# Performance work log

Hardware: AMD Instinct MI355X
Metric: run time of the kernel (lower is better)

Reference implementation:

```python
import jax, jax.numpy as jnp
import numpy as np

WIN_SIZE = 256           # GlobalConfig.win_size (assumed)
NFFT = 2 * WIN_SIZE      # 512 -> NFREQ = 257 rfft bins
HOP = WIN_SIZE
NFREQ = WIN_SIZE + 1
K = 3                    # all kernel sizes in the model
EPS = 1e-5


def _stft(x):
    # x: (B, S) -> (B, T, F, 2) real view of complex STFT (hann window, no center)
    B, S = x.shape
    T = (S - NFFT) // HOP + 1
    n = jnp.arange(NFFT)
    win = 0.5 - 0.5 * jnp.cos(2.0 * jnp.pi * n / NFFT)
    idx = jnp.arange(T)[:, None] * HOP + n[None, :]
    frames = x[:, idx] * win                       # (B, T, NFFT)
    spec = jnp.fft.rfft(frames, axis=-1)           # (B, T, F) complex
    return jnp.stack([spec.real, spec.imag], axis=-1).astype(x.dtype)


def _td_layer(x, W, b, same):
    # time-distributed conv over the frequency axis. x: (B,T,F,Cin), W: (k,Cin,Cout)
    k = W.shape[0]
    if same:
        x = jnp.pad(x, ((0, 0), (0, 0), (k // 2, k - 1 - k // 2), (0, 0)))
    Fout = x.shape[2] - k + 1
    xs = jnp.stack([x[:, :, i:i + Fout] for i in range(k)], axis=0)  # (k,B,T,Fout,Cin)
    return jnp.einsum('kbtfc,kco->btfo', xs, W) + b


def _td_block(x, W1, b1, W2, b2):
    h = jax.nn.relu(_td_layer(x, W1, b1, True))
    return _td_layer(h, W2, b2, True)


def _layer(x, g, beta, dw, W1, b1, W2, b2):
    # LayerNorm over (F, C), causal depthwise conv over T, TD pointwise block, ReLU
    B, T, F, C = x.shape
    mu = x.mean(axis=(-2, -1), keepdims=True)
    var = x.var(axis=(-2, -1), keepdims=True)
    xn = (x - mu) * jax.lax.rsqrt(var + EPS) * g + beta
    h = xn.reshape(B, T, F * C)
    hp = jnp.pad(h, ((0, 0), (K - 1, 0), (0, 0)))   # causal left-pad on time
    y = sum(hp[:, i:i + T, :] * dw[:, i] for i in range(K))  # (B,T,F*C) depthwise
    y = y.reshape(B, T, F, C)
    return jax.nn.relu(_td_block(y, W1, b1, W2, b2))


def setup_inputs() -> dict:
    key = jax.random.key(0)
    ks = iter(jax.random.split(key, 40))
    def rn(shape, s=0.05):
        return (jax.random.normal(next(ks), shape) * s).astype(jnp.float32)
    F = NFREQ
    d = {}
    d['x'] = jax.random.normal(next(ks), (8, 262144), dtype=jnp.float32)
    d['l0_W1'] = rn((3, 2, 4)); d['l0_b1'] = jnp.zeros((4,), jnp.float32)
    d['l0_W2'] = rn((3, 4, 8)); d['l0_b2'] = jnp.zeros((8,), jnp.float32)
    for name, cin in (('l1', 8), ('l2', 16), ('l3', 24)):
        d[name + '_g'] = jnp.ones((F, cin), jnp.float32)
        d[name + '_bn'] = jnp.zeros((F, cin), jnp.float32)
        d[name + '_dw'] = rn((F * cin, 3), 0.3)
        d[name + '_W1'] = rn((3, cin, 8)); d[name + '_b1'] = jnp.zeros((8,), jnp.float32)
        d[name + '_W2'] = rn((3, 8, 8)); d[name + '_b2'] = jnp.zeros((8,), jnp.float32)
    d['fc1_W'] = rn((3, 32, 1)); d['fc1_b'] = jnp.zeros((1,), jnp.float32)
    d['fc2_W'] = rn((F - 2, 1)); d['fc2_b'] = jnp.zeros((1,), jnp.float32)
    return d


def reference(x, l0_W1, l0_b1, l0_W2, l0_b2,
              l1_g, l1_bn, l1_dw, l1_W1, l1_b1, l1_W2, l1_b2,
              l2_g, l2_bn, l2_dw, l2_W1, l2_b1, l2_W2, l2_b2,
              l3_g, l3_bn, l3_dw, l3_W1, l3_b1, l3_W2, l3_b2,
              fc1_W, fc1_b, fc2_W, fc2_b):
    s = _stft(x)                                            # (B,T,F,2)
    h = jax.nn.relu(_td_block(s, l0_W1, l0_b1, l0_W2, l0_b2))  # (B,T,F,8)
    h = jnp.concatenate([h, _layer(h, l1_g, l1_bn, l1_dw, l1_W1, l1_b1, l1_W2, l1_b2)], axis=3)
    h = jnp.concatenate([h, _layer(h, l2_g, l2_bn, l2_dw, l2_W1, l2_b1, l2_W2, l2_b2)], axis=3)
    h = jnp.concatenate([h, _layer(h, l3_g, l3_bn, l3_dw, l3_W1, l3_b1, l3_W2, l3_b2)], axis=3)
    h = jax.nn.relu(_td_layer(h, fc1_W, fc1_b, False))[..., 0]  # (B,T,F-2)
    out = jax.nn.sigmoid(h @ fc2_W + fc2_b)                 # (B,T,1)
    return out[..., 0]                                      # (B,T)
```

## Files before the change

### kernel.cpp

```cpp
#include <hip/hip_runtime.h>
#include <hip/hip_fp16.h>

namespace {

constexpr int BATCH = 8;
constexpr int SLEN  = 262144;
constexpr int TT    = 1023;
constexpr int NF    = 257;
constexpr int NCH   = 24;
constexpr int NBT   = BATCH * TT;
constexpr int FRS   = NCH * NF;
constexpr float EPS = 1e-5f;

typedef _Float16 h2v __attribute__((ext_vector_type(2)));

__device__ inline float fdot2(unsigned a, unsigned b, float c) {
#if __has_builtin(__builtin_amdgcn_fdot2)
  return __builtin_amdgcn_fdot2(__builtin_bit_cast(h2v, a),
                                __builtin_bit_cast(h2v, b), c, false);
#else
  h2v av = __builtin_bit_cast(h2v, a), bv = __builtin_bit_cast(h2v, b);
  return fmaf((float)av[0], (float)bv[0], fmaf((float)av[1], (float)bv[1], c));
#endif
}
__device__ inline unsigned packh2(float a, float b) {
  h2v v; v[0] = (_Float16)a; v[1] = (_Float16)b;
  return __builtin_bit_cast(unsigned, v);
}
__device__ inline unsigned short f2h(float v) {
  return __builtin_bit_cast(unsigned short, (_Float16)v);
}
__device__ inline __half2 u2h(unsigned u) { return __builtin_bit_cast(__half2, u); }
__device__ inline int div257(int e) { return (e * 65282) >> 24; }

__global__ __launch_bounds__(256, 8) void stft_l0_kernel(
    const float* __restrict__ x,
    const float* __restrict__ W1g, const float* __restrict__ b1g,
    const float* __restrict__ W2g, const float* __restrict__ b2g,
    __half* __restrict__ H, float* __restrict__ stats0)
{
  __shared__ float  xw[512];
  __shared__ __align__(16) float2 abE[128];
  __shared__ __align__(16) float2 abO[128];
  __shared__ float2 oxc[128];
  __shared__ float  sre[NF + 2];
  __shared__ float  sim[NF + 2];
  __shared__ float  h1[4][NF + 2];
  __shared__ float  wW1[24], wb1[4], wW2[96], wb2[8];
  __shared__ float  red[8];

  const int tid = threadIdx.x;
  const int bt  = blockIdx.x;
  const int b   = bt / TT;
  const int t   = bt - b * TT;
  const float* xp = x + (size_t)b * SLEN + (size_t)t * 256;

  if (tid < 24) wW1[tid] = W1g[tid];
  if (tid < 4)  wb1[tid] = b1g[tid];
  if (tid < 96) wW2[tid] = W2g[tid];
  if (tid < 8)  wb2[tid] = b2g[tid];

  const float STEP = 6.283185307179586f / 512.0f;
  for (int n = tid; n < 512; n += 256) {
    float sv, cv;
    sincosf(STEP * (float)n, &sv, &cv);
    xw[n] = xp[n] * (0.5f - 0.5f * cv);
  }
  __syncthreads();

  if (tid < 128) {
    const int n = 2 * tid;
    abE[tid] = (n == 0) ? make_float2(0.f, 0.f)
                        : make_float2(xw[n] + xw[512 - n], xw[n] - xw[512 - n]);
  } else {
    const int n = 2 * (tid - 128) + 1;
    abO[tid - 128] = make_float2(xw[n] + xw[512 - n], xw[n] - xw[512 - n]);
  }
  __syncthreads();

  const float x0 = xw[0], x256 = xw[256];
  {
    const int  k = tid & 127;
    const bool P = (tid >= 128);
    float s1, c1;
    sincosf(STEP * (float)k, &s1, &c1);
    const float c2 = fmaf(c1,c1,-s1*s1), s2 = 2.f*c1*s1;
    const float c3 = fmaf(c2,c1,-s2*s1), s3 = fmaf(c2,s1, s2*c1);
    const float c4 = fmaf(c2,c2,-s2*s2), s4 = 2.f*c2*s2;
    const float c5 = fmaf(c4,c1,-s4*s1), s5 = fmaf(c4,s1, s4*c1);
    const float c6 = fmaf(c4,c2,-s4*s2), s6 = fmaf(c4,s2, s4*c2);
    const float c7 = fmaf(c4,c3,-s4*s3), s7 = fmaf(c4,s3, s4*c3);
    const float c8 = fmaf(c4,c4,-s4*s4), s8 = 2.f*c4*s4;
    float cA = P ? c1 : 1.f, sA = P ? s1 : 0.f;
    float cB = P ? c3 : c2,  sB = P ? s3 : s2;
    float cC = P ? c5 : c4,  sC = P ? s5 : s4;
    float cD = P ? c7 : c6,  sD = P ? s7 : s6;
    const float4* ab4 = P ? (const float4*)abO : (const float4*)abE;
    float re = 0.f, im = 0.f;
    for (int m = 0; m < 32; ++m) {
      const float4 q0 = ab4[2*m];
      const float4 q1 = ab4[2*m + 1];
      re = fmaf(q0.x, cA, re); im = fmaf(q0.y, sA, im);
      re = fmaf(q0.z, cB, re); im = fmaf(q0.w, sB, im);
      re = fmaf(q1.x, cC, re); im = fmaf(q1.y, sC, im);
      re = fmaf(q1.z, cD, re); im = fmaf(q1.w, sD, im);
      float t0;
      t0 = fmaf(cA, c8, -sA*s8); sA = fmaf(cA, s8, sA*c8); cA = t0;
      t0 = fmaf(cB, c8, -sB*s8); sB = fmaf(cB, s8, sB*c8); cB = t0;
      t0 = fmaf(cC, c8, -sC*s8); sC = fmaf(cC, s8, sC*c8); cC = t0;
      t0 = fmaf(cD, c8, -sD*s8); sD = fmaf(cD, s8, sD*c8); cD = t0;
    }
    if (P) oxc[k] = make_float2(re, im);

    float tr = 0.f, ti = 0.f;
    if (tid & 1) {
      const float v = abO[tid >> 1].y;
      ti = ((tid >> 1) & 1) ? v : -v;
    } else {
      const float v = abE[tid >> 1].x;
      tr = ((tid >> 1) & 1) ? -v : v;
    }
    #pragma unroll
    for (int off = 32; off > 0; off >>= 1) {
      tr += __shfl_down(tr, off, 64);
      ti += __shfl_down(ti, off, 64);
    }
    if ((tid & 63) == 0) { red[(tid >> 6)*2] = tr; red[(tid >> 6)*2 + 1] = ti; }
    __syncthreads();

    if (!P) {
      const float rb  = x0 + ((k & 1) ? -x256 : x256);
      const float reo = oxc[k].x, imo = oxc[k].y;
      sre[1 + k]       = rb + re + reo;
      sim[1 + k]       = -(im + imo);
      sre[1 + 256 - k] = rb + re - reo;
      sim[1 + 256 - k] = im - imo;
    }
    if (tid == 0) {
      sre[1 + 128] = x0 + x256 + red[0] + red[2] + red[4] + red[6];
      sim[1 + 128] = red[1] + red[3] + red[5] + red[7];
      sre[0] = 0.f; sim[0] = 0.f; sre[258] = 0.f; sim[258] = 0.f;
    }
  }
  __syncthreads();

  for (int f = tid; f < NF; f += 256) {
    float acc[4] = {wb1[0], wb1[1], wb1[2], wb1[3]};
    #pragma unroll
    for (int i = 0; i < 3; ++i) {
      float vr = sre[f + i], vi = sim[f + i];
      #pragma unroll
      for (int c = 0; c < 4; ++c)
        acc[c] = fmaf(vr, wW1[(i*2+0)*4 + c], fmaf(vi, wW1[(i*2+1)*4 + c], acc[c]));
    }
    #pragma unroll
    for (int c = 0; c < 4; ++c) h1[c][f + 1] = fmaxf(acc[c], 0.f);
  }
  if (tid < 4) { h1[tid][0] = 0.f; h1[tid][NF + 1] = 0.f; }
  __syncthreads();

  const size_t obase = (size_t)bt * FRS;
  float ps1 = 0.f, ps2 = 0.f;
  for (int f = tid; f < NF; f += 256) {
    float acc[8];
    #pragma unroll
    for (int c = 0; c < 8; ++c) acc[c] = wb2[c];
    #pragma unroll
    for (int i = 0; i < 3; ++i)
      #pragma unroll
      for (int c4 = 0; c4 < 4; ++c4) {
        float hv = h1[c4][f + i];
        #pragma unroll
        for (int c = 0; c < 8; ++c)
          acc[c] = fmaf(hv, wW2[(i*4+c4)*8 + c], acc[c]);
      }
    #pragma unroll
    for (int c = 0; c < 8; ++c) {
      const __half hv = __float2half(fmaxf(acc[c], 0.f));
      H[obase + (size_t)c * NF + f] = hv;
      const float v = __half2float(hv);
      ps1 += v;
      ps2 = fmaf(v, v, ps2);
    }
  }
  #pragma unroll
  for (int off = 32; off > 0; off >>= 1) {
    ps1 += __shfl_down(ps1, off, 64);
    ps2 += __shfl_down(ps2, off, 64);
  }
  __syncthreads();
  if ((tid & 63) == 0) { red[(tid >> 6) * 2] = ps1; red[(tid >> 6) * 2 + 1] = ps2; }
  __syncthreads();
  if (tid == 0) {
    stats0[bt * 2]     = red[0] + red[2] + red[4] + red[6];
    stats0[bt * 2 + 1] = red[1] + red[3] + red[5] + red[7];
  }
}

__device__ inline void fold_one(int idx, int CIN,
    const float* g, const float* bn, const float* dw, __half* dst, int NEL) {
  const int c = div257(idx), f = idx - c * 257;
  const int s = f * CIN + c;
  const float gv = g[s], bv = bn[s];
  const float d0 = dw[s*3], d1 = dw[s*3+1], d2 = dw[s*3+2];
  dst[idx]         = __float2half(gv * d0);
  dst[NEL + idx]   = __float2half(gv * d1);
  dst[2*NEL + idx] = __float2half(gv * d2);
  dst[3*NEL + idx] = __float2half(bv * (d0 + d1 + d2));
  dst[4*NEL + idx] = __float2half(bv * (d1 + d2));
  dst[5*NEL + idx] = __float2half(bv * d2);
}

__global__ __launch_bounds__(256) void fold_all(
    const float* g1, const float* bn1, const float* dw1, __half* t1,
    const float* g2, const float* bn2, const float* dw2, __half* t2,
    const float* g3, const float* bn3, const float* dw3, __half* t3)
{
  int idx = blockIdx.x * 256 + threadIdx.x;
  if (idx < 8*257) { fold_one(idx, 8, g1, bn1, dw1, t1, 8*257); return; }
  idx -= 8*257;
  if (idx < 16*257) { fold_one(idx, 16, g2, bn2, dw2, t2, 16*257); return; }
  idx -= 16*257;
  if (idx < 24*257) fold_one(idx, 24, g3, bn3, dw3, t3, 24*257);
}

template<int CIN, bool HEAD>
__global__ __launch_bounds__(256, 8) void layer_bt(
    const __half* __restrict__ H, __half* __restrict__ Hout,
    const float* __restrict__ st0, const float* __restrict__ st1,
    const float* __restrict__ st2, float* __restrict__ stats_out,
    const __half* __restrict__ tbl,
    const float* __restrict__ W1g, const float* __restrict__ b1g,
    const float* __restrict__ W2g, const float* __restrict__ b2g,
    const float* __restrict__ fc1W, const float* __restrict__ fc1b,
    const float* __restrict__ fc2W, const float* __restrict__ fc2b,
    float* __restrict__ out)
{
  constexpr int NEL   = CIN * NF;
  constexpr int NP2   = NEL / 2;
  constexpr int NPER2 = (NP2 + 255) / 256;
  constexpr int TAIL2 = NP2 - 256 * (NPER2 - 1);
  constexpr int PC1   = CIN + 2;
  constexpr int PC2   = 10;
  constexpr int NQ1   = CIN / 2;

  __shared__ unsigned short y_t[259 * PC1];
  __shared__ unsigned short h1_t[259 * PC2];
  __shared__ unsigned w1p[3 * NQ1 * 8];
  __shared__ unsigned w2p[96];
  __shared__ float wb1[8], wb2[8];
  __shared__ float red[8];
  __shared__ unsigned wfc1p[HEAD ? 48 : 1];

  const int tid = threadIdx.x;
  const int bt  = blockIdx.x;
  const int b   = bt / TT;
  const int t   = bt - b * TT;

  for (int idx = tid; idx < 3 * NQ1 * 8; idx += 256) {
    const int o = idx & 7, q = (idx >> 3) % NQ1, i = idx / (NQ1 * 8);
    w1p[idx] = packh2(W1g[(i*CIN + 2*q)*8 + o], W1g[(i*CIN + 2*q + 1)*8 + o]);
  }
  if (tid < 96) {
    const int o = tid & 7, q = (tid >> 3) & 3, i = tid >> 5;
    w2p[tid] = packh2(W2g[(i*8 + 2*q)*8 + o], W2g[(i*8 + 2*q + 1)*8 + o]);
  }
  if (tid < 8) { wb1[tid] = b1g[tid]; wb2[tid] = b2g[tid]; }
  if (tid < PC1) { y_t[tid] = 0; y_t[258*PC1 + tid] = 0; }
  if (tid < PC2) { h1_t[tid] = 0; h1_t[258*PC2 + tid] = 0; }
  if constexpr (HEAD) {
    if (tid < 48) {
      const int q = tid & 15, i = tid >> 4;
      wfc1p[tid] = packh2(fc1W[i*32 + 2*q], fc1W[i*32 + 2*q + 1]);
    }
  }

  float mu0 = 0.f, rs0 = 0.f, mu1 = 0.f, rs1 = 0.f, mu2, rs2;
  {
    const float inv = 1.0f / (float)NEL;
    float s1 = st0[bt*2], s2v = st0[bt*2+1];
    if constexpr (CIN >= 16) { s1 += st1[bt*2]; s2v += st1[bt*2+1]; }
    if constexpr (CIN >= 24) { s1 += st2[bt*2]; s2v += st2[bt*2+1]; }
    mu2 = s1 * inv; rs2 = rsqrtf(s2v * inv - mu2*mu2 + EPS);
    if (t >= 1) {
      const int fb = bt - 1;
      float a = st0[fb*2], c = st0[fb*2+1];
      if constexpr (CIN >= 16) { a += st1[fb*2]; c += st1[fb*2+1]; }
      if constexpr (CIN >= 24) { a += st2[fb*2]; c += st2[fb*2+1]; }
      mu1 = a * inv; rs1 = rsqrtf(c * inv - mu1*mu1 + EPS);
    }
    if (t >= 2) {
      const int fb = bt - 2;
      float a = st0[fb*2], c = st0[fb*2+1];
      if constexpr (CIN >= 16) { a += st1[fb*2]; c += st1[fb*2+1]; }
      if constexpr (CIN >= 24) { a += st2[fb*2]; c += st2[fb*2+1]; }
      mu0 = a * inv; rs0 = rsqrtf(c * inv - mu0*mu0 + EPS);
    }
  }
  const __half2 rs0h = __float2half2_rn(rs0);
  const __half2 rs1h = __float2half2_rn(rs1);
  const __half2 rs2h = __float2half2_rn(rs2);
  const __half2 nm0h = __float2half2_rn(-mu0);
  const __half2 nm1h = __float2half2_rn(-mu1);
  const __half2 nm2h = __float2half2_rn(-mu2);

  const int base = b * TT;
  const unsigned* F2 = (const unsigned*)(H + (size_t)bt * FRS);
  const unsigned* F1 = (const unsigned*)(H + (size_t)max(bt - 1, base) * FRS);
  const unsigned* F0 = (const unsigned*)(H + (size_t)max(bt - 2, base) * FRS);
  const unsigned* P0 = (const unsigned*)tbl;
  const unsigned* P1 = (const unsigned*)(tbl + NEL);
  const unsigned* P2 = (const unsigned*)(tbl + 2 * NEL);
  const int qsel = (t >= 2) ? 0 : (t == 1 ? 1 : 2);
  const unsigned* Qp = (const unsigned*)(tbl + (3 + qsel) * NEL);

  #pragma unroll
  for (int j = 0; j < NPER2; ++j) {
    const bool act = (j < NPER2 - 1) || (tid < TAIL2);
    if (act) {
      const int p  = tid + 256 * j;
      const int e0 = 2 * p;
      const int c0 = div257(e0);
      const int fi = e0 - c0 * 257;
      const __half2 rp0 = __hmul2(rs0h, u2h(P0[p]));
      const __half2 rp1 = __hmul2(rs1h, u2h(P1[p]));
      const __half2 rp2 = __hmul2(rs2h, u2h(P2[p]));
      __half2 acc = __hfma2(nm0h, rp0, u2h(Qp[p]));
      acc = __hfma2(nm1h, rp1, acc);
      acc = __hfma2(nm2h, rp2, acc);
      acc = __hfma2(u2h(F0[p]), rp0, acc);
      acc = __hfma2(u2h(F1[p]), rp1, acc);
      acc = __hfma2(u2h(F2[p]), rp2, acc);
      const unsigned r = __builtin_bit_cast(unsigned, acc);
      const int a1 = (fi + 1) * PC1 + c0;
      y_t[a1] = (unsigned short)(r & 0xffffu);
      const int a2 = (fi == 256) ? (PC1 + c0 + 1) : (a1 + PC1);
      y_t[a2] = (unsigned short)(r >> 16);
    }
  }
  __syncthreads();

  {
    const int f = tid;
    float acc[8];
    #pragma unroll
    for (int c = 0; c < 8; ++c) acc[c] = wb1[c];
    const unsigned* yw = (const unsigned*)y_t;
    #pragma unroll
    for (int i = 0; i < 3; ++i) {
      const unsigned* row = yw + (f + i) * (PC1 / 2);
      for (int q = 0; q < NQ1; ++q) {
        const unsigned yv = row[q];
        #pragma unroll
        for (int c = 0; c < 8; ++c)
          acc[c] = fdot2(yv, w1p[(i * NQ1 + q) * 8 + c], acc[c]);
      }
    }
    unsigned* hw = (unsigned*)h1_t + (f + 1) * (PC2 / 2);
    #pragma unroll
    for (int k = 0; k < 4; ++k)
      hw[k] = packh2(fmaxf(acc[2*k], 0.f), fmaxf(acc[2*k+1], 0.f));
  }
  if (tid < 8) {
    float a = wb1[tid];
    const unsigned* yw = (const unsigned*)y_t;
    #pragma unroll
    for (int i = 0; i < 3; ++i) {
      const unsigned* row = yw + (256 + i) * (PC1 / 2);
      for (int q = 0; q < NQ1; ++q)
        a = fdot2(row[q], w1p[(i * NQ1 + q) * 8 + tid], a);
    }
    h1_t[257 * PC2 + tid] = f2h(fmaxf(a, 0.f));
  }
  __syncthreads();

  float ps1 = 0.f, ps2 = 0.f;
  {
    const int f = tid;
    float o2[8];
    #pragma unroll
    for (int c = 0; c < 8; ++c) o2[c] = wb2[c];
    const unsigned* hw = (const unsigned*)h1_t;
    #pragma unroll
    for (int i = 0; i < 3; ++i) {
      const unsigned* row = hw + (f + i) * (PC2 / 2);
      #pragma unroll
      for (int q = 0; q < 4; ++q) {
        const unsigned hv = row[q];
        #pragma unroll
        for (int c = 0; c < 8; ++c)
          o2[c] = fdot2(hv, w2p[(i*4 + q)*8 + c], o2[c]);
      }
    }
    if constexpr (!HEAD) {
      const size_t ob = (size_t)bt * FRS + (size_t)CIN * NF;
      #pragma unroll
      for (int c = 0; c < 8; ++c) {
        const __half hv = __float2half(fmaxf(o2[c], 0.f));
        Hout[ob + (size_t)c * NF + f] = hv;
        const float v = __half2float(hv);
        ps1 += v;
        ps2 = fmaf(v, v, ps2);
      }
    } else {
      unsigned* ow = (unsigned*)y_t + f * (PC1 / 2);
      #pragma unroll
      for (int k = 0; k < 4; ++k)
        ow[k] = packh2(fmaxf(o2[2*k], 0.f), fmaxf(o2[2*k+1], 0.f));
    }
  }
  if (tid >= 8 && tid < 16) {
    const int c8 = tid - 8;
    float a = wb2[c8];
    const unsigned* hw = (const unsigned*)h1_t;
    #pragma unroll
    for (int i = 0; i < 3; ++i) {
      const unsigned* row = hw + (256 + i) * (PC2 / 2);
      #pragma unroll
      for (int q = 0; q < 4; ++q)
        a = fdot2(row[q], w2p[(i*4 + q)*8 + c8], a);
    }
    if constexpr (!HEAD) {
      const size_t ob = (size_t)bt * FRS + (size_t)CIN * NF;
      const __half hv = __float2half(fmaxf(a, 0.f));
      Hout[ob + (size_t)c8 * NF + 256] = hv;
      const float v = __half2float(hv);
      ps1 += v;
      ps2 = fmaf(v, v, ps2);
    } else {
      y_t[256 * PC1 + c8] = f2h(fmaxf(a, 0.f));
    }
  }

  if constexpr (!HEAD) {
    #pragma unroll
    for (int off = 32; off > 0; off >>= 1) {
      ps1 += __shfl_down(ps1, off, 64);
      ps2 += __shfl_down(ps2, off, 64);
    }
    if ((tid & 63) == 0) { red[(tid >> 6)*2] = ps1; red[(tid >> 6)*2+1] = ps2; }
    __syncthreads();
    if (tid == 0) {
      stats_out[bt*2]     = red[0] + red[2] + red[4] + red[6];
      stats_out[bt*2 + 1] = red[1] + red[3] + red[5] + red[7];
    }
  } else {
    __syncthreads();
    float part = 0.f;
    if (tid < NF - 2) {
      const unsigned short* xgu = (const unsigned short*)F2;
      float acc = fc1b[0];
      #pragma unroll
      for (int i = 0; i < 3; ++i) {
        const int pos = tid + i;
        for (int q = 0; q < 12; ++q) {
          const unsigned lo = xgu[(2*q) * 257 + pos];
          const unsigned hi = xgu[(2*q + 1) * 257 + pos];
          acc = fdot2(lo | (hi << 16), wfc1p[i*16 + q], acc);
        }
        const unsigned* orow = (const unsigned*)y_t + pos * (PC1 / 2);
        #pragma unroll
        for (int q = 0; q < 4; ++q)
          acc = fdot2(orow[q], wfc1p[i*16 + 12 + q], acc);
      }
      part = fmaxf(acc, 0.f) * fc2W[tid];
    }
    #pragma unroll
    for (int off = 32; off > 0; off >>= 1) part += __shfl_down(part, off, 64);
    if ((tid & 63) == 0) red[tid >> 6] = part;
    __syncthreads();
    if (tid == 0) {
      const float tot = red[0] + red[1] + red[2] + red[3] + fc2b[0];
      out[bt] = 1.0f / (1.0f + expf(-tot));
    }
  }
}

}

extern "C" void kernel_launch(void* const* d_in, const int* in_sizes, int n_in,
                              void* d_out, int out_size, void* d_ws, size_t ws_size,
                              hipStream_t stream) {
  (void)in_sizes; (void)n_in; (void)out_size; (void)ws_size;
  const float* x = (const float*)d_in[0];
  float* out = (float*)d_out;
  char*  wsb = (char*)d_ws;

  __half* H   = (__half*)wsb;
  char* p = wsb + (size_t)NBT * FRS * sizeof(__half);
  float* st0  = (float*)p; p += 2 * NBT * sizeof(float);
  float* st1  = (float*)p; p += 2 * NBT * sizeof(float);
  float* st2  = (float*)p; p += 2 * NBT * sizeof(float);
  __half* tbl1 = (__half*)p; p += 6 * (8  * NF) * sizeof(__half);
  __half* tbl2 = (__half*)p; p += 6 * (16 * NF) * sizeof(__half);
  __half* tbl3 = (__half*)p;

  dim3 blk(256);

  fold_all<<<dim3((48 * 257 + 255) / 256), blk, 0, stream>>>(
      (const float*)d_in[5],  (const float*)d_in[6],  (const float*)d_in[7],  tbl1,
      (const float*)d_in[12], (const float*)d_in[13], (const float*)d_in[14], tbl2,
      (const float*)d_in[19], (const float*)d_in[20], (const float*)d_in[21], tbl3);

  stft_l0_kernel<<<dim3(NBT), blk, 0, stream>>>(
      x, (const float*)d_in[1], (const float*)d_in[2],
      (const float*)d_in[3], (const float*)d_in[4], H, st0);

  layer_bt<8, false><<<dim3(NBT), blk, 0, stream>>>(
      H, H, st0, nullptr, nullptr, st1, tbl1,
      (const float*)d_in[8], (const float*)d_in[9],
      (const float*)d_in[10], (const float*)d_in[11],
      nullptr, nullptr, nullptr, nullptr, nullptr);

  layer_bt<16, false><<<dim3(NBT), blk, 0, stream>>>(
      H, H, st0, st1, nullptr, st2, tbl2,
      (const float*)d_in[15], (const float*)d_in[16],
      (const float*)d_in[17], (const float*)d_in[18],
      nullptr, nullptr, nullptr, nullptr, nullptr);

  layer_bt<24, true><<<dim3(NBT), blk, 0, stream>>>(
      H, nullptr, st0, st1, st2, nullptr, tbl3,
      (const float*)d_in[22], (const float*)d_in[23],
      (const float*)d_in[24], (const float*)d_in[25],
      (const float*)d_in[26], (const float*)d_in[27],
      (const float*)d_in[28], (const float*)d_in[29],
      out);
}
```

Measured before the change: 409.2 us.

## Pad activation rows to 264 and interleave fold tables into uint4 records

Activation rows in the workspace are padded from 257 to 264 halves per channel, so every half2 pair stays within one channel row. This drops the cross-row special case and lets the channel index come from a cheap divide by 132. The folded LayerNorm/depthwise coefficients are packed into one uint4 per pair, plus side arrays used only for the first two time steps, so the main loop issues one wide table load instead of four scattered ones. In exchange the workspace grows about 3%, and every producer must write zeros into the padding columns.

```diff
diff --git a/kernel.cpp b/kernel.cpp
--- a/kernel.cpp
+++ b/kernel.cpp
@@ -7,9 +7,11 @@
 constexpr int SLEN  = 262144;
 constexpr int TT    = 1023;
 constexpr int NF    = 257;
+constexpr int RL    = 264;
 constexpr int NCH   = 24;
 constexpr int NBT   = BATCH * TT;
-constexpr int FRS   = NCH * NF;
+constexpr int FRS   = NCH * RL;
+constexpr int PPR   = RL / 2;
 constexpr float EPS = 1e-5f;
 
 typedef _Float16 h2v __attribute__((ext_vector_type(2)));
@@ -31,7 +33,7 @@
   return __builtin_bit_cast(unsigned short, (_Float16)v);
 }
 __device__ inline __half2 u2h(unsigned u) { return __builtin_bit_cast(__half2, u); }
-__device__ inline int div257(int e) { return (e * 65282) >> 24; }
+__device__ inline int div132(int p) { return (p * 993) >> 17; }
 
 __global__ __launch_bounds__(256, 8) void stft_l0_kernel(
     const float* __restrict__ x,
@@ -177,11 +179,15 @@
     #pragma unroll
     for (int c = 0; c < 8; ++c) {
       const __half hv = __float2half(fmaxf(acc[c], 0.f));
-      H[obase + (size_t)c * NF + f] = hv;
+      H[obase + (size_t)c * RL + f] = hv;
       const float v = __half2float(hv);
       ps1 += v;
       ps2 = fmaf(v, v, ps2);
     }
+  }
+  if (tid < 56) {
+    const int c = tid / 7, f = 257 + tid - 7 * (tid / 7);
+    H[obase + (size_t)c * RL + f] = __float2half(0.f);
   }
   #pragma unroll
   for (int off = 32; off > 0; off >>= 1) {
@@ -197,31 +203,45 @@
   }
 }
 
-__device__ inline void fold_one(int idx, int CIN,
-    const float* g, const float* bn, const float* dw, __half* dst, int NEL) {
-  const int c = div257(idx), f = idx - c * 257;
-  const int s = f * CIN + c;
-  const float gv = g[s], bv = bn[s];
-  const float d0 = dw[s*3], d1 = dw[s*3+1], d2 = dw[s*3+2];
-  dst[idx]         = __float2half(gv * d0);
-  dst[NEL + idx]   = __float2half(gv * d1);
-  dst[2*NEL + idx] = __float2half(gv * d2);
-  dst[3*NEL + idx] = __float2half(bv * (d0 + d1 + d2));
-  dst[4*NEL + idx] = __float2half(bv * (d1 + d2));
-  dst[5*NEL + idx] = __float2half(bv * d2);
+__device__ inline void fold_pair(int p, int CIN,
+    const float* g, const float* bn, const float* dw,
+    uint4* TI, unsigned* Q1s, unsigned* Q2s)
+{
+  const int c = p / PPR, fp = p - PPR * c;
+  float P0[2], P1[2], P2[2], Q0[2], Q1[2], Q2[2];
+  #pragma unroll
+  for (int h = 0; h < 2; ++h) {
+    const int f = 2 * fp + h;
+    if (f < NF) {
+      const int s = f * CIN + c;
+      const float gv = g[s], bv = bn[s];
+      const float d0 = dw[s*3], d1 = dw[s*3+1], d2 = dw[s*3+2];
+      P0[h] = gv * d0; P1[h] = gv * d1; P2[h] = gv * d2;
+      Q0[h] = bv * (d0 + d1 + d2); Q1[h] = bv * (d1 + d2); Q2[h] = bv * d2;
+    } else {
+      P0[h] = P1[h] = P2[h] = Q0[h] = Q1[h] = Q2[h] = 0.f;
+    }
+  }
+  TI[p] = make_uint4(packh2(P0[0], P0[1]), packh2(P1[0], P1[1]),
+                     packh2(P2[0], P2[1]), packh2(Q0[0], Q0[1]));
+  Q1s[p] = packh2(Q1[0], Q1[1]);
+  Q2s[p] = packh2(Q2[0], Q2[1]);
 }
 
 __global__ __launch_bounds__(256) void fold_all(
-    const float* g1, const float* bn1, const float* dw1, __half* t1,
-    const float* g2, const float* bn2, const float* dw2, __half* t2,
-    const float* g3, const float* bn3, const float* dw3, __half* t3)
+    const float* g1, const float* bn1, const float* dw1,
+    uint4* T1, unsigned* Q1a, unsigned* Q2a,
+    const float* g2, const float* bn2, const float* dw2,
+    uint4* T2, unsigned* Q1b, unsigned* Q2b,
+    const float* g3, const float* bn3, const float* dw3,
+    uint4* T3, unsigned* Q1c, unsigned* Q2c)
 {
-  int idx = blockIdx.x * 256 + threadIdx.x;
-  if (idx < 8*257) { fold_one(idx, 8, g1, bn1, dw1, t1, 8*257); return; }
-  idx -= 8*257;
-  if (idx < 16*257) { fold_one(idx, 16, g2, bn2, dw2, t2, 16*257); return; }
-  idx -= 16*257;
-  if (idx < 24*257) fold_one(idx, 24, g3, bn3, dw3, t3, 24*257);
+  int p = blockIdx.x * 256 + threadIdx.x;
+  if (p < 8 * PPR) { fold_pair(p, 8, g1, bn1, dw1, T1, Q1a, Q2a); return; }
+  p -= 8 * PPR;
+  if (p < 16 * PPR) { fold_pair(p, 16, g2, bn2, dw2, T2, Q1b, Q2b); return; }
+  p -= 16 * PPR;
+  if (p < 24 * PPR) fold_pair(p, 24, g3, bn3, dw3, T3, Q1c, Q2c);
 }
 
 template<int CIN, bool HEAD>
@@ -229,7 +249,8 @@
     const __half* __restrict__ H, __half* __restrict__ Hout,
     const float* __restrict__ st0, const float* __restrict__ st1,
     const float* __restrict__ st2, float* __restrict__ stats_out,
-    const __half* __restrict__ tbl,
+    const uint4* __restrict__ TI,
+    const unsigned* __restrict__ Q1s, const unsigned* __restrict__ Q2s,
     const float* __restrict__ W1g, const float* __restrict__ b1g,
     const float* __restrict__ W2g, const float* __restrict__ b2g,
     const float* __restrict__ fc1W, const float* __restrict__ fc1b,
@@ -237,14 +258,13 @@
     float* __restrict__ out)
 {
   constexpr int NEL   = CIN * NF;
-  constexpr int NP2   = NEL / 2;
-  constexpr int NPER2 = (NP2 + 255) / 256;
-  constexpr int TAIL2 = NP2 - 256 * (NPER2 - 1);
+  constexpr int NPAIR = CIN * PPR;
+  constexpr int NJ    = (NPAIR + 255) / 256;
   constexpr int PC1   = CIN + 2;
   constexpr int PC2   = 10;
   constexpr int NQ1   = CIN / 2;
 
-  __shared__ unsigned short y_t[259 * PC1];
+  __shared__ unsigned short y_t[265 * PC1];
   __shared__ unsigned short h1_t[259 * PC2];
   __shared__ unsigned w1p[3 * NQ1 * 8];
   __shared__ unsigned w2p[96];
@@ -266,7 +286,7 @@
     w2p[tid] = packh2(W2g[(i*8 + 2*q)*8 + o], W2g[(i*8 + 2*q + 1)*8 + o]);
   }
   if (tid < 8) { wb1[tid] = b1g[tid]; wb2[tid] = b2g[tid]; }
-  if (tid < PC1) { y_t[tid] = 0; y_t[258*PC1 + tid] = 0; }
+  if (tid < PC1) y_t[tid] = 0;
   if (tid < PC2) { h1_t[tid] = 0; h1_t[258*PC2 + tid] = 0; }
   if constexpr (HEAD) {
     if (tid < 48) {
@@ -308,34 +328,33 @@
   const unsigned* F2 = (const unsigned*)(H + (size_t)bt * FRS);
   const unsigned* F1 = (const unsigned*)(H + (size_t)max(bt - 1, base) * FRS);
   const unsigned* F0 = (const unsigned*)(H + (size_t)max(bt - 2, base) * FRS);
-  const unsigned* P0 = (const unsigned*)tbl;
-  const unsigned* P1 = (const unsigned*)(tbl + NEL);
-  const unsigned* P2 = (const unsigned*)(tbl + 2 * NEL);
-  const int qsel = (t >= 2) ? 0 : (t == 1 ? 1 : 2);
-  const unsigned* Qp = (const unsigned*)(tbl + (3 + qsel) * NEL);
+  const bool useSide = (t < 2);
+  const unsigned* Qside = (t == 1) ? Q1s : Q2s;
 
   #pragma unroll
-  for (int j = 0; j < NPER2; ++j) {
-    const bool act = (j < NPER2 - 1) || (tid < TAIL2);
+  for (int j = 0; j < NJ; ++j) {
+    const int p = tid + 256 * j;
+    const bool act = (j < NJ - 1) || (p < NPAIR);
     if (act) {
-      const int p  = tid + 256 * j;
-      const int e0 = 2 * p;
-      const int c0 = div257(e0);
-      const int fi = e0 - c0 * 257;
-      const __half2 rp0 = __hmul2(rs0h, u2h(P0[p]));
-      const __half2 rp1 = __hmul2(rs1h, u2h(P1[p]));
-      const __half2 rp2 = __hmul2(rs2h, u2h(P2[p]));
-      __half2 acc = __hfma2(nm0h, rp0, u2h(Qp[p]));
+      const uint4 T = TI[p];
+      unsigned qw = T.w;
+      if (useSide) qw = Qside[p];
+      const unsigned x0 = F0[p], x1 = F1[p], x2 = F2[p];
+      const __half2 rp0 = __hmul2(rs0h, u2h(T.x));
+      const __half2 rp1 = __hmul2(rs1h, u2h(T.y));
+      const __half2 rp2 = __hmul2(rs2h, u2h(T.z));
+      __half2 acc = __hfma2(nm0h, rp0, u2h(qw));
       acc = __hfma2(nm1h, rp1, acc);
       acc = __hfma2(nm2h, rp2, acc);
-      acc = __hfma2(u2h(F0[p]), rp0, acc);
-      acc = __hfma2(u2h(F1[p]), rp1, acc);
-      acc = __hfma2(u2h(F2[p]), rp2, acc);
+      acc = __hfma2(u2h(x0), rp0, acc);
+      acc = __hfma2(u2h(x1), rp1, acc);
+      acc = __hfma2(u2h(x2), rp2, acc);
       const unsigned r = __builtin_bit_cast(unsigned, acc);
-      const int a1 = (fi + 1) * PC1 + c0;
-      y_t[a1] = (unsigned short)(r & 0xffffu);
-      const int a2 = (fi == 256) ? (PC1 + c0 + 1) : (a1 + PC1);
-      y_t[a2] = (unsigned short)(r >> 16);
+      const int c = div132(p);
+      const int f = 2 * (p - PPR * c);
+      const int a = (f + 1) * PC1 + c;
+      y_t[a]       = (unsigned short)(r & 0xffffu);
+      y_t[a + PC1] = (unsigned short)(r >> 16);
     }
   }
   __syncthreads();
@@ -393,11 +412,11 @@
       }
     }
     if constexpr (!HEAD) {
-      const size_t ob = (size_t)bt * FRS + (size_t)CIN * NF;
+      const size_t ob = (size_t)bt * FRS + (size_t)CIN * RL;
       #pragma unroll
       for (int c = 0; c < 8; ++c) {
         const __half hv = __float2half(fmaxf(o2[c], 0.f));
-        Hout[ob + (size_t)c * NF + f] = hv;
+        Hout[ob + (size_t)c * RL + f] = hv;
         const float v = __half2float(hv);
         ps1 += v;
         ps2 = fmaf(v, v, ps2);
@@ -421,14 +440,22 @@
         a = fdot2(row[q], w2p[(i*4 + q)*8 + c8], a);
     }
     if constexpr (!HEAD) {
-      const size_t ob = (size_t)bt * FRS + (size_t)CIN * NF;
+      const size_t ob = (size_t)bt * FRS + (size_t)CIN * RL;
       const __half hv = __float2half(fmaxf(a, 0.f));
-      Hout[ob + (size_t)c8 * NF + 256] = hv;
+      Hout[ob + (size_t)c8 * RL + 256] = hv;
       const float v = __half2float(hv);
       ps1 += v;
       ps2 = fmaf(v, v, ps2);
     } else {
       y_t[256 * PC1 + c8] = f2h(fmaxf(a, 0.f));
+    }
+  }
+  if constexpr (!HEAD) {
+    if (tid >= 64 && tid < 120) {
+      const size_t ob = (size_t)bt * FRS + (size_t)CIN * RL;
+      const int i2 = tid - 64;
+      const int c = i2 / 7, f = 257 + i2 - 7 * (i2 / 7);
+      Hout[ob + (size_t)c * RL + f] = __float2half(0.f);
     }
   }
 
@@ -454,8 +481,8 @@
       for (int i = 0; i < 3; ++i) {
         const int pos = tid + i;
         for (int q = 0; q < 12; ++q) {
-          const unsigned lo = xgu[(2*q) * 257 + pos];
-          const unsigned hi = xgu[(2*q + 1) * 257 + pos];
+          const unsigned lo = xgu[(2*q) * RL + pos];
+          const unsigned hi = xgu[(2*q + 1) * RL + pos];
           acc = fdot2(lo | (hi << 16), wfc1p[i*16 + q], acc);
         }
         const unsigned* orow = (const unsigned*)y_t + pos * (PC1 / 2);
@@ -486,40 +513,49 @@
   float* out = (float*)d_out;
   char*  wsb = (char*)d_ws;
 
-  __half* H   = (__half*)wsb;
+  __half* H = (__half*)wsb;
   char* p = wsb + (size_t)NBT * FRS * sizeof(__half);
-  float* st0  = (float*)p; p += 2 * NBT * sizeof(float);
-  float* st1  = (float*)p; p += 2 * NBT * sizeof(float);
-  float* st2  = (float*)p; p += 2 * NBT * sizeof(float);
-  __half* tbl1 = (__half*)p; p += 6 * (8  * NF) * sizeof(__half);
-  __half* tbl2 = (__half*)p; p += 6 * (16 * NF) * sizeof(__half);
-  __half* tbl3 = (__half*)p;
+  float* st0 = (float*)p; p += 2 * NBT * sizeof(float);
+  float* st1 = (float*)p; p += 2 * NBT * sizeof(float);
+  float* st2 = (float*)p; p += 2 * NBT * sizeof(float);
+  uint4*    T1  = (uint4*)p;    p += (size_t)(8  * PPR) * 16;
+  unsigned* Q1a = (unsigned*)p; p += (size_t)(8  * PPR) * 4;
+  unsigned* Q2a = (unsigned*)p; p += (size_t)(8  * PPR) * 4;
+  uint4*    T2  = (uint4*)p;    p += (size_t)(16 * PPR) * 16;
+  unsigned* Q1b = (unsigned*)p; p += (size_t)(16 * PPR) * 4;
+  unsigned* Q2b = (unsigned*)p; p += (size_t)(16 * PPR) * 4;
+  uint4*    T3  = (uint4*)p;    p += (size_t)(24 * PPR) * 16;
+  unsigned* Q1c = (unsigned*)p; p += (size_t)(24 * PPR) * 4;
+  unsigned* Q2c = (unsigned*)p;
 
   dim3 blk(256);
 
-  fold_all<<<dim3((48 * 257 + 255) / 256), blk, 0, stream>>>(
-      (const float*)d_in[5],  (const float*)d_in[6],  (const float*)d_in[7],  tbl1,
-      (const float*)d_in[12], (const float*)d_in[13], (const float*)d_in[14], tbl2,
-      (const float*)d_in[19], (const float*)d_in[20], (const float*)d_in[21], tbl3);
+  fold_all<<<dim3((48 * PPR + 255) / 256), blk, 0, stream>>>(
+      (const float*)d_in[5],  (const float*)d_in[6],  (const float*)d_in[7],
+      T1, Q1a, Q2a,
+      (const float*)d_in[12], (const float*)d_in[13], (const float*)d_in[14],
+      T2, Q1b, Q2b,
+      (const float*)d_in[19], (const float*)d_in[20], (const float*)d_in[21],
+      T3, Q1c, Q2c);
 
   stft_l0_kernel<<<dim3(NBT), blk, 0, stream>>>(
       x, (const float*)d_in[1], (const float*)d_in[2],
       (const float*)d_in[3], (const float*)d_in[4], H, st0);
 
   layer_bt<8, false><<<dim3(NBT), blk, 0, stream>>>(
-      H, H, st0, nullptr, nullptr, st1, tbl1,
+      H, H, st0, nullptr, nullptr, st1, T1, Q1a, Q2a,
       (const float*)d_in[8], (const float*)d_in[9],
       (const float*)d_in[10], (const float*)d_in[11],
       nullptr, nullptr, nullptr, nullptr, nullptr);
 
   layer_bt<16, false><<<dim3(NBT), blk, 0, stream>>>(
-      H, H, st0, st1, nullptr, st2, tbl2,
+      H, H, st0, st1, nullptr, st2, T2, Q1b, Q2b,
       (const float*)d_in[15], (const float*)d_in[16],
       (const float*)d_in[17], (const float*)d_in[18],
       nullptr, nullptr, nullptr, nullptr, nullptr);
 
   layer_bt<24, true><<<dim3(NBT), blk, 0, stream>>>(
-      H, nullptr, st0, st1, st2, nullptr, tbl3,
+      H, nullptr, st0, st1, st2, nullptr, T3, Q1c, Q2c,
       (const float*)d_in[22], (const float*)d_in[23],
       (const float*)d_in[24], (const float*)d_in[25],
       (const float*)d_in[26], (const float*)d_in[27],
```

New measurement: 431.4 us. 1.05x slower.
